# Kernel tuning notes

Measured on AMD Instinct MI355X. Metric: run time of the kernel, lower is better.

The kernel has to match this reference:

```python
import jax, jax.numpy as jnp
import numpy as np

HIDDEN = 1024
HEADS = 16
HEAD = HIDDEN // HEADS


def setup_inputs() -> dict:
    key = jax.random.key(0)
    k1, k2, k3, k4, k5, k6 = jax.random.split(key, 6)
    B, S = 2, 2048
    x = jax.random.normal(k1, (B, S, HIDDEN), dtype=jnp.float32)
    mask = jax.random.randint(k2, (B, S), 0, 2, dtype=jnp.int32)
    # torch nn.Linear params: W [out,in], b [out]
    s = 1.0 / np.sqrt(HIDDEN)
    qkv_w = jax.random.uniform(k3, (3 * HIDDEN, HIDDEN), jnp.float32, -s, s)
    qkv_b = jax.random.uniform(k4, (3 * HIDDEN,), jnp.float32, -s, s)
    out_w = jax.random.uniform(k5, (HIDDEN, HIDDEN), jnp.float32, -s, s)
    out_b = jax.random.uniform(k6, (HIDDEN,), jnp.float32, -s, s)
    return {"x": x, "mask": mask, "qkv_w": qkv_w, "qkv_b": qkv_b,
            "out_w": out_w, "out_b": out_b}


def reference(x, mask, qkv_w, qkv_b, out_w, out_b):
    B, S, H = x.shape
    scale = HEAD ** -0.5
    qkv = x @ qkv_w.T + qkv_b                      # [B,S,3H]
    qkv = qkv.reshape(B, S, 3, HEADS, HEAD)
    qkv = jnp.transpose(qkv, (2, 0, 3, 1, 4))      # [3,B,h,S,d]
    q, k, v = qkv[0], qkv[1], qkv[2]
    scores = jnp.einsum('bhqd,bhkd->bhqk', q, k) * scale
    # key-padding mask [B,S] -> [B,1,1,S]
    scores = jnp.where(mask[:, None, None, :] == 0, -1e9, scores)
    attn = jax.nn.softmax(scores, axis=-1)
    # dropout is identity in eval mode
    ctx = jnp.einsum('bhqk,bhkd->bhqd', attn, v)   # [B,h,S,d]
    ctx = jnp.transpose(ctx, (0, 2, 1, 3)).reshape(B, S, H)
    return ctx @ out_w.T + out_b
```

## Files before the change

kernel.cpp:

```cpp
#include <hip/hip_runtime.h>
#include <hip/hip_bf16.h>

#define S_LEN 2048
#define NH    16
#define HD    64
#define HID   1024
#define BATCH 2
#define STK   72
#define SCQ   0.18033688f

typedef __bf16 bf16x8 __attribute__((ext_vector_type(8)));
typedef float  f32x4  __attribute__((ext_vector_type(4)));

__device__ __forceinline__ unsigned int pk2(float lo, float hi) {
    union { __hip_bfloat162 h; unsigned int u; } c;
    c.h = __float22bfloat162_rn(make_float2(lo, hi));
    return c.u;
}
__device__ __forceinline__ uint4 pk8(float4 a, float4 b) {
    uint4 o;
    o.x = pk2(a.x, a.y); o.y = pk2(a.z, a.w);
    o.z = pk2(b.x, b.y); o.w = pk2(b.z, b.w);
    return o;
}
__device__ __forceinline__ float exp2_hw(float x) {
    float r; asm("v_exp_f32 %0, %1" : "=v"(r) : "v"(x)); return r;
}
__device__ __forceinline__ void gll16(const unsigned short* g, unsigned short* l) {
    __builtin_amdgcn_global_load_lds(
        (const __attribute__((address_space(1))) void*)g,
        (__attribute__((address_space(3))) void*)l, 16, 0, 0);
}

__global__ __launch_bounds__(256)
void fill_constf(float* __restrict__ out, long n, float v) {
    long i = (long)blockIdx.x * 256 + threadIdx.x;
    const long stride = (long)gridDim.x * 256;
    for (; i < n; i += stride) out[i] = v;
}

__global__ __launch_bounds__(256)
void cvt_bf16(const float* __restrict__ src, unsigned short* __restrict__ dst, long n8) {
    long t = (long)blockIdx.x * 256 + threadIdx.x;
    const long stride = (long)gridDim.x * 256;
    for (; t < n8; t += stride) {
        const float4 a = *(const float4*)(src + t * 8);
        const float4 b = *(const float4*)(src + t * 8 + 4);
        *(uint4*)(dst + t * 8) = pk8(a, b);
    }
}
__global__ __launch_bounds__(256)
void cvt2_bf16(const float* __restrict__ s0, unsigned short* __restrict__ d0, long n0,
               const float* __restrict__ s1, unsigned short* __restrict__ d1, long n1) {
    long t = (long)blockIdx.x * 256 + threadIdx.x;
    const long stride = (long)gridDim.x * 256;
    for (; t < n0 + n1; t += stride) {
        const float* s; unsigned short* d; long i;
        if (t < n0) { s = s0; d = d0; i = t; } else { s = s1; d = d1; i = t - n0; }
        const float4 a = *(const float4*)(s + i * 8);
        const float4 b = *(const float4*)(s + i * 8 + 4);
        *(uint4*)(d + i * 8) = pk8(a, b);
    }
}

__global__ __launch_bounds__(256)
void gemm_bf16(const unsigned short* __restrict__ A,
               const unsigned short* __restrict__ W,
               const float* __restrict__ bias,
               unsigned short* __restrict__ o0,
               unsigned short* __restrict__ o1,
               unsigned short* __restrict__ o2,
               float* __restrict__ of,
               int mode)
{
    __shared__ __align__(16) unsigned short lA[3][128 * 32];
    __shared__ __align__(16) unsigned short lB[3][128 * 32];
    const int tid  = threadIdx.x;
    const int lane = tid & 63, wv = tid >> 6;
    const int quad = lane >> 4, l16 = lane & 15;
    const int wm = (wv & 1) * 64, wn = (wv >> 1) * 64;

    const int nwg = gridDim.x * gridDim.y;
    const int bid = blockIdx.y * gridDim.x + blockIdx.x;
    const int xcd = bid & 7, boff = bid >> 3;
    const int qd = nwg >> 3, rm = nwg & 7;
    const int swz = (xcd < rm ? xcd * (qd + 1) : rm * (qd + 1) + (xcd - rm) * qd) + boff;
    const int m0 = (swz / gridDim.x) * 128, n0 = (swz % gridDim.x) * 128;

    f32x4 acc[4][4] = {};

    const int srow0 = wv * 32 + (lane >> 2);
    const int srow1 = srow0 + 16;
    const int csrc  = ((lane & 3) ^ ((lane >> 3) & 3)) * 8;
    const unsigned short* pa0 = A + (long)(m0 + srow0) * HID + csrc;
    const unsigned short* pa1 = A + (long)(m0 + srow1) * HID + csrc;
    const unsigned short* pb0 = W + (long)(n0 + srow0) * HID + csrc;
    const unsigned short* pb1 = W + (long)(n0 + srow1) * HID + csrc;

    const int cq8 = (quad ^ ((l16 >> 1) & 3)) * 8;

#define STAGE_G(bufi, koff)                                        \
    do {                                                           \
        gll16(pa0 + (koff), &lA[bufi][(wv * 2 + 0) * 512]);        \
        gll16(pa1 + (koff), &lA[bufi][(wv * 2 + 1) * 512]);        \
        gll16(pb0 + (koff), &lB[bufi][(wv * 2 + 0) * 512]);        \
        gll16(pb1 + (koff), &lB[bufi][(wv * 2 + 1) * 512]);        \
    } while (0)

    STAGE_G(0, 0);
    STAGE_G(1, 32);

    int cur = 0;
    for (int k0 = 0; k0 < HID; k0 += 32) {
        if (k0 + 32 < HID) { asm volatile("s_waitcnt vmcnt(4)" ::: "memory"); }
        else               { asm volatile("s_waitcnt vmcnt(0)" ::: "memory"); }
        __builtin_amdgcn_s_barrier();
        asm volatile("" ::: "memory");

        if (k0 + 64 < HID) {
            const int nxt = cur ? cur - 1 : 2;
            STAGE_G(nxt, k0 + 64);
        }

        bf16x8 af[4], bfr[4];
#pragma unroll
        for (int mt = 0; mt < 4; mt++)
            af[mt] = *(const bf16x8*)&lA[cur][(wm + mt * 16 + l16) * 32 + cq8];
#pragma unroll
        for (int nt = 0; nt < 4; nt++)
            bfr[nt] = *(const bf16x8*)&lB[cur][(wn + nt * 16 + l16) * 32 + cq8];
#pragma unroll
        for (int mt = 0; mt < 4; mt++)
#pragma unroll
            for (int nt = 0; nt < 4; nt++)
                acc[mt][nt] = __builtin_amdgcn_mfma_f32_16x16x32_bf16(
                    af[mt], bfr[nt], acc[mt][nt], 0, 0, 0);

        cur = (cur < 2) ? cur + 1 : 0;
    }
#undef STAGE_G

    if (mode == 0) {
#pragma unroll
        for (int nt = 0; nt < 4; nt++) {
            const int n = n0 + wn + nt * 16 + l16;
            const float bv = bias[n];
            const int part = n >> 10, f = n & 1023, h = f >> 6, d = f & 63;
#pragma unroll
            for (int mt = 0; mt < 4; mt++) {
                const int mbase = m0 + wm + mt * 16 + quad * 4;
                const int b = mbase >> 11, s0 = mbase & 2047;
                const int bh = b * NH + h;
                if (part == 2) {
                    uint2 o;
                    o.x = pk2(acc[mt][nt][0] + bv, acc[mt][nt][1] + bv);
                    o.y = pk2(acc[mt][nt][2] + bv, acc[mt][nt][3] + bv);
                    *(uint2*)&o2[((long)bh * HD + d) * S_LEN + s0] = o;
                } else {
                    unsigned short* dst = (part == 0) ? o0 : o1;
                    const float qsc = (part == 0) ? SCQ : 1.0f;
#pragma unroll
                    for (int r = 0; r < 4; r++) {
                        union { __hip_bfloat16 h; unsigned short u; } cv;
                        cv.h = __float2bfloat16((acc[mt][nt][r] + bv) * qsc);
                        dst[((long)bh * S_LEN + s0 + r) * HD + d] = cv.u;
                    }
                }
            }
        }
    } else {
#pragma unroll
        for (int nt = 0; nt < 4; nt++) {
            const int n = n0 + wn + nt * 16 + l16;
            const float bv = bias[n];
#pragma unroll
            for (int mt = 0; mt < 4; mt++) {
                const int mbase = m0 + wm + mt * 16 + quad * 4;
#pragma unroll
                for (int r = 0; r < 4; r++)
                    of[(long)(mbase + r) * HID + n] = acc[mt][nt][r] + bv;
            }
        }
    }
}

__global__ __launch_bounds__(512)
void attn(const unsigned short* __restrict__ q,
          const unsigned short* __restrict__ k,
          const unsigned short* __restrict__ vt_g,
          const int* __restrict__ mask,
          unsigned short* __restrict__ ctx)
{
    __shared__ __align__(16) unsigned short kt[2][64 * STK];
    __shared__ __align__(16) unsigned short vt[2][64 * STK];
    __shared__ __align__(16) __bf16 pt[8][16 * 72];
    __shared__ float mkv[2][64];

    const int tid  = threadIdx.x;
    const int lane = tid & 63, wv = tid >> 6;
    const int quad = lane >> 4, l16 = lane & 15;
    const int qt = blockIdx.x, h = blockIdx.y, b = blockIdx.z;
    const int bh = b * NH + h;

    const int sq = qt * 128 + wv * 16 + l16;
    bf16x8 qf0 = *(const bf16x8*)&q[((long)bh * S_LEN + sq) * HD + quad * 8];
    bf16x8 qf1 = *(const bf16x8*)&q[((long)bh * S_LEN + sq) * HD + 32 + quad * 8];

    float mrun = -1e30f, lrun = 0.f;
    f32x4 Of[4] = {};

    const int sr = tid >> 3, sc8 = (tid & 7) * 8;
    const unsigned short* kg = k    + ((long)bh * S_LEN + sr) * HD + sc8;
    const unsigned short* vg = vt_g + ((long)bh * HD + sr) * S_LEN + sc8;
    __bf16* ptw = pt[wv];

    uint4 rk = *(const uint4*)(kg);
    uint4 rv = *(const uint4*)(vg);
    float rm = 0.f;
    if (tid < 64) rm = (mask[b * S_LEN + tid] == 0) ? -1e9f : 0.f;
    *(uint4*)&kt[0][sr * STK + sc8] = rk;
    *(uint4*)&vt[0][sr * STK + sc8] = rv;
    if (tid < 64) mkv[0][tid] = rm;
    rk = *(const uint4*)(kg + (long)64 * HD);
    rv = *(const uint4*)(vg + 64);
    if (tid < 64) rm = (mask[b * S_LEN + 64 + tid] == 0) ? -1e9f : 0.f;
    asm volatile("s_waitcnt lgkmcnt(0)" ::: "memory");
    __builtin_amdgcn_s_barrier();
    asm volatile("" ::: "memory");

    for (int k0 = 0; k0 < S_LEN; k0 += 64) {
        const int cur = (k0 >> 6) & 1;
        if (k0 + 64 < S_LEN) {
            *(uint4*)&kt[cur ^ 1][sr * STK + sc8] = rk;
            *(uint4*)&vt[cur ^ 1][sr * STK + sc8] = rv;
            if (tid < 64) mkv[cur ^ 1][tid] = rm;
            if (k0 + 128 < S_LEN) {
                rk = *(const uint4*)(kg + (long)(k0 + 128) * HD);
                rv = *(const uint4*)(vg + (k0 + 128));
                if (tid < 64) rm = (mask[b * S_LEN + k0 + 128 + tid] == 0) ? -1e9f : 0.f;
            }
        }

        float st[4][4];
#pragma unroll
        for (int nt = 0; nt < 4; nt++) {
            bf16x8 k0f = *(const bf16x8*)&kt[cur][(nt * 16 + l16) * STK + quad * 8];
            bf16x8 k1f = *(const bf16x8*)&kt[cur][(nt * 16 + l16) * STK + 32 + quad * 8];
            const float4 mv = *(const float4*)&mkv[cur][nt * 16 + quad * 4];
            f32x4 s = {mv.x, mv.y, mv.z, mv.w};
            s = __builtin_amdgcn_mfma_f32_16x16x32_bf16(k0f, qf0, s, 0, 0, 0);
            s = __builtin_amdgcn_mfma_f32_16x16x32_bf16(k1f, qf1, s, 0, 0, 0);
#pragma unroll
            for (int r = 0; r < 4; r++) st[nt][r] = s[r];
        }

        float mxa[4];
#pragma unroll
        for (int nt = 0; nt < 4; nt++)
            mxa[nt] = fmaxf(fmaxf(st[nt][0], st[nt][1]), fmaxf(st[nt][2], st[nt][3]));
        float mx = fmaxf(fmaxf(mxa[0], mxa[1]), fmaxf(mxa[2], mxa[3]));
        mx = fmaxf(mx, __shfl_xor(mx, 16, 64));
        mx = fmaxf(mx, __shfl_xor(mx, 32, 64));

        if (!__all(mx <= mrun + 8.f)) {
            const float mn = fmaxf(mrun, mx);
            const float alpha = exp2_hw(mrun - mn);
#pragma unroll
            for (int nt = 0; nt < 4; nt++) Of[nt] *= alpha;
            lrun *= alpha;
            mrun = mn;
        }

        float pr[4][4];
#pragma unroll
        for (int nt = 0; nt < 4; nt++)
#pragma unroll
            for (int r = 0; r < 4; r++) pr[nt][r] = exp2_hw(st[nt][r] - mrun);
        float rsa[4];
#pragma unroll
        for (int nt = 0; nt < 4; nt++)
            rsa[nt] = (pr[nt][0] + pr[nt][1]) + (pr[nt][2] + pr[nt][3]);
        float rs = (rsa[0] + rsa[1]) + (rsa[2] + rsa[3]);
        rs += __shfl_xor(rs, 16, 64);
        rs += __shfl_xor(rs, 32, 64);
        lrun += rs;

#pragma unroll
        for (int nt = 0; nt < 4; nt++) {
            const unsigned long long lo = pk2(pr[nt][0], pr[nt][1]);
            const unsigned long long hi = pk2(pr[nt][2], pr[nt][3]);
            *(unsigned long long*)&ptw[l16 * 72 + nt * 16 + quad * 4] = lo | (hi << 32);
        }
        asm volatile("" ::: "memory");

#pragma unroll
        for (int ks = 0; ks < 2; ks++) {
            bf16x8 bp = *(const bf16x8*)&ptw[l16 * 72 + ks * 32 + quad * 8];
#pragma unroll
            for (int nt = 0; nt < 4; nt++) {
                bf16x8 av = *(const bf16x8*)&vt[cur][(nt * 16 + l16) * STK + ks * 32 + quad * 8];
                Of[nt] = __builtin_amdgcn_mfma_f32_16x16x32_bf16(av, bp, Of[nt], 0, 0, 0);
            }
        }

        asm volatile("s_waitcnt lgkmcnt(0)" ::: "memory");
        __builtin_amdgcn_s_barrier();
        asm volatile("" ::: "memory");
    }

    const float inv = 1.f / lrun;
#pragma unroll
    for (int nt = 0; nt < 4; nt++) {
        uint2 o;
        o.x = pk2(Of[nt][0] * inv, Of[nt][1] * inv);
        o.y = pk2(Of[nt][2] * inv, Of[nt][3] * inv);
        *(uint2*)&ctx[((long)b * S_LEN + sq) * HID + h * HD + nt * 16 + quad * 4] = o;
    }
}

extern "C" void kernel_launch(void* const* d_in, const int* in_sizes, int n_in,
                              void* d_out, int out_size, void* d_ws, size_t ws_size,
                              hipStream_t stream) {
    float* outp = (float*)d_out;

    const float* x = nullptr; const int* mask = nullptr;
    const float* qkv_w = nullptr; const float* qkv_b = nullptr;
    const float* out_w = nullptr; const float* out_b = nullptr;
    for (int i = 0; i < n_in; i++) {
        switch (in_sizes[i]) {
            case 4194304: x     = (const float*)d_in[i]; break;
            case 4096:    mask  = (const int*)d_in[i];   break;
            case 3145728: qkv_w = (const float*)d_in[i]; break;
            case 3072:    qkv_b = (const float*)d_in[i]; break;
            case 1048576: out_w = (const float*)d_in[i]; break;
            case 1024:    out_b = (const float*)d_in[i]; break;
            default: break;
        }
    }
    if (!x || !mask || !qkv_w || !qkv_b || !out_w || !out_b) {
        fill_constf<<<256, 256, 0, stream>>>(outp, (long)out_size, 1000.0f);
        return;
    }

    const size_t per = (size_t)BATCH * NH * S_LEN * HD;
    const size_t nx  = (size_t)BATCH * S_LEN * HID;
    const size_t nqw = (size_t)3 * HID * HID;
    const size_t now = (size_t)HID * HID;
    if (ws_size < 4 * per * sizeof(unsigned short)) {
        fill_constf<<<256, 256, 0, stream>>>(outp, (long)out_size, 2000.0f);
        return;
    }

    unsigned short* wsq = (unsigned short*)d_ws;
    unsigned short* wsk = wsq + per;
    unsigned short* wsv = wsk + per;
    unsigned short* wsc = wsv + per;
    unsigned short* xb  = wsc;
    unsigned short* qwb = (unsigned short*)d_out;
    unsigned short* owb = wsq;

    cvt2_bf16<<<1024, 256, 0, stream>>>(x, xb, (long)(nx / 8), qkv_w, qwb, (long)(nqw / 8));
    gemm_bf16<<<dim3(3 * HID / 128, BATCH * S_LEN / 128), 256, 0, stream>>>(
        xb, qwb, qkv_b, wsq, wsk, wsv, nullptr, 0);
    attn<<<dim3(S_LEN / 128, NH, BATCH), 512, 0, stream>>>(wsq, wsk, wsv, mask, wsc);
    cvt_bf16<<<512, 256, 0, stream>>>(out_w, owb, (long)(now / 8));
    gemm_bf16<<<dim3(HID / 128, BATCH * S_LEN / 128), 256, 0, stream>>>(
        wsc, owb, out_b, nullptr, nullptr, nullptr, outp, 1);
}
```

Before: 231.4 us.

## Store Q transposed, defer softmax row-sum reduction, add MFMA priority hints

The QKV projection epilogue now writes Q transposed ([bh, d, s]) with packed 8-byte stores, like V, instead of scattered 2-byte stores. The attention kernel gathers Q fragments with strided scalar loads once per block. Inside the attention loop the per-row sum is kept as partial per-lane sums and cross-lane shuffled only once at the end, and the max shuffle runs only when a rescale is needed. The MFMA sections are wrapped in s_setprio. Together these aim to cut epilogue store cost and loop shuffle overhead, at the cost of uncoalesced strided Q loads.

```diff
diff --git a/kernel.cpp b/kernel.cpp
--- a/kernel.cpp
+++ b/kernel.cpp
@@ -151,19 +151,19 @@
                 const int mbase = m0 + wm + mt * 16 + quad * 4;
                 const int b = mbase >> 11, s0 = mbase & 2047;
                 const int bh = b * NH + h;
-                if (part == 2) {
+                if (part != 1) {
+                    const float qsc = (part == 0) ? SCQ : 1.0f;
+                    unsigned short* dst = (part == 0) ? o0 : o2;
                     uint2 o;
-                    o.x = pk2(acc[mt][nt][0] + bv, acc[mt][nt][1] + bv);
-                    o.y = pk2(acc[mt][nt][2] + bv, acc[mt][nt][3] + bv);
-                    *(uint2*)&o2[((long)bh * HD + d) * S_LEN + s0] = o;
+                    o.x = pk2((acc[mt][nt][0] + bv) * qsc, (acc[mt][nt][1] + bv) * qsc);
+                    o.y = pk2((acc[mt][nt][2] + bv) * qsc, (acc[mt][nt][3] + bv) * qsc);
+                    *(uint2*)&dst[((long)bh * HD + d) * S_LEN + s0] = o;
                 } else {
-                    unsigned short* dst = (part == 0) ? o0 : o1;
-                    const float qsc = (part == 0) ? SCQ : 1.0f;
 #pragma unroll
                     for (int r = 0; r < 4; r++) {
                         union { __hip_bfloat16 h; unsigned short u; } cv;
-                        cv.h = __float2bfloat16((acc[mt][nt][r] + bv) * qsc);
-                        dst[((long)bh * S_LEN + s0 + r) * HD + d] = cv.u;
+                        cv.h = __float2bfloat16(acc[mt][nt][r] + bv);
+                        o1[((long)bh * S_LEN + s0 + r) * HD + d] = cv.u;
                     }
                 }
             }
@@ -203,10 +203,18 @@
     const int bh = b * NH + h;
 
     const int sq = qt * 128 + wv * 16 + l16;
-    bf16x8 qf0 = *(const bf16x8*)&q[((long)bh * S_LEN + sq) * HD + quad * 8];
-    bf16x8 qf1 = *(const bf16x8*)&q[((long)bh * S_LEN + sq) * HD + 32 + quad * 8];
-
-    float mrun = -1e30f, lrun = 0.f;
+
+    const unsigned short* qtg = q + (long)bh * HD * S_LEN + sq;
+    union { unsigned short u[8]; bf16x8 v; } qu0, qu1;
+#pragma unroll
+    for (int j = 0; j < 8; j++) {
+        qu0.u[j] = qtg[(long)(quad * 8 + j) * S_LEN];
+        qu1.u[j] = qtg[(long)(32 + quad * 8 + j) * S_LEN];
+    }
+    const bf16x8 qf0 = qu0.v, qf1 = qu1.v;
+
+    float mrun = -1e30f;
+    float lsum = 0.f;
     f32x4 Of[4] = {};
 
     const int sr = tid >> 3, sc8 = (tid & 7) * 8;
@@ -216,14 +224,14 @@
 
     uint4 rk = *(const uint4*)(kg);
     uint4 rv = *(const uint4*)(vg);
-    float rm = 0.f;
-    if (tid < 64) rm = (mask[b * S_LEN + tid] == 0) ? -1e9f : 0.f;
+    float rmv = 0.f;
+    if (tid < 64) rmv = (mask[b * S_LEN + tid] == 0) ? -1e9f : 0.f;
     *(uint4*)&kt[0][sr * STK + sc8] = rk;
     *(uint4*)&vt[0][sr * STK + sc8] = rv;
-    if (tid < 64) mkv[0][tid] = rm;
+    if (tid < 64) mkv[0][tid] = rmv;
     rk = *(const uint4*)(kg + (long)64 * HD);
     rv = *(const uint4*)(vg + 64);
-    if (tid < 64) rm = (mask[b * S_LEN + 64 + tid] == 0) ? -1e9f : 0.f;
+    if (tid < 64) rmv = (mask[b * S_LEN + 64 + tid] == 0) ? -1e9f : 0.f;
     asm volatile("s_waitcnt lgkmcnt(0)" ::: "memory");
     __builtin_amdgcn_s_barrier();
     asm volatile("" ::: "memory");
@@ -233,15 +241,16 @@
         if (k0 + 64 < S_LEN) {
             *(uint4*)&kt[cur ^ 1][sr * STK + sc8] = rk;
             *(uint4*)&vt[cur ^ 1][sr * STK + sc8] = rv;
-            if (tid < 64) mkv[cur ^ 1][tid] = rm;
+            if (tid < 64) mkv[cur ^ 1][tid] = rmv;
             if (k0 + 128 < S_LEN) {
                 rk = *(const uint4*)(kg + (long)(k0 + 128) * HD);
                 rv = *(const uint4*)(vg + (k0 + 128));
-                if (tid < 64) rm = (mask[b * S_LEN + k0 + 128 + tid] == 0) ? -1e9f : 0.f;
+                if (tid < 64) rmv = (mask[b * S_LEN + k0 + 128 + tid] == 0) ? -1e9f : 0.f;
             }
         }
 
         float st[4][4];
+        __builtin_amdgcn_s_setprio(1);
 #pragma unroll
         for (int nt = 0; nt < 4; nt++) {
             bf16x8 k0f = *(const bf16x8*)&kt[cur][(nt * 16 + l16) * STK + quad * 8];
@@ -253,21 +262,22 @@
 #pragma unroll
             for (int r = 0; r < 4; r++) st[nt][r] = s[r];
         }
+        __builtin_amdgcn_s_setprio(0);
 
         float mxa[4];
 #pragma unroll
         for (int nt = 0; nt < 4; nt++)
             mxa[nt] = fmaxf(fmaxf(st[nt][0], st[nt][1]), fmaxf(st[nt][2], st[nt][3]));
-        float mx = fmaxf(fmaxf(mxa[0], mxa[1]), fmaxf(mxa[2], mxa[3]));
-        mx = fmaxf(mx, __shfl_xor(mx, 16, 64));
-        mx = fmaxf(mx, __shfl_xor(mx, 32, 64));
-
-        if (!__all(mx <= mrun + 8.f)) {
+        const float pmax = fmaxf(fmaxf(mxa[0], mxa[1]), fmaxf(mxa[2], mxa[3]));
+
+        if (__any(pmax > mrun + 8.f)) {
+            float mx = fmaxf(pmax, __shfl_xor(pmax, 16, 64));
+            mx = fmaxf(mx, __shfl_xor(mx, 32, 64));
             const float mn = fmaxf(mrun, mx);
             const float alpha = exp2_hw(mrun - mn);
 #pragma unroll
             for (int nt = 0; nt < 4; nt++) Of[nt] *= alpha;
-            lrun *= alpha;
+            lsum *= alpha;
             mrun = mn;
         }
 
@@ -280,10 +290,7 @@
 #pragma unroll
         for (int nt = 0; nt < 4; nt++)
             rsa[nt] = (pr[nt][0] + pr[nt][1]) + (pr[nt][2] + pr[nt][3]);
-        float rs = (rsa[0] + rsa[1]) + (rsa[2] + rsa[3]);
-        rs += __shfl_xor(rs, 16, 64);
-        rs += __shfl_xor(rs, 32, 64);
-        lrun += rs;
+        lsum += (rsa[0] + rsa[1]) + (rsa[2] + rsa[3]);
 
 #pragma unroll
         for (int nt = 0; nt < 4; nt++) {
@@ -293,6 +300,7 @@
         }
         asm volatile("" ::: "memory");
 
+        __builtin_amdgcn_s_setprio(1);
 #pragma unroll
         for (int ks = 0; ks < 2; ks++) {
             bf16x8 bp = *(const bf16x8*)&ptw[l16 * 72 + ks * 32 + quad * 8];
@@ -302,13 +310,16 @@
                 Of[nt] = __builtin_amdgcn_mfma_f32_16x16x32_bf16(av, bp, Of[nt], 0, 0, 0);
             }
         }
+        __builtin_amdgcn_s_setprio(0);
 
         asm volatile("s_waitcnt lgkmcnt(0)" ::: "memory");
         __builtin_amdgcn_s_barrier();
         asm volatile("" ::: "memory");
     }
 
-    const float inv = 1.f / lrun;
+    float lt = lsum + __shfl_xor(lsum, 16, 64);
+    lt += __shfl_xor(lt, 32, 64);
+    const float inv = 1.f / lt;
 #pragma unroll
     for (int nt = 0; nt < 4; nt++) {
         uint2 o;
```

After: 225.5 us. 1.03x faster.
